# Optimization experiments

Hardware: AMD Instinct MI355X
Metric: run time of the kernel (lower is better)

## Reference

```python
import jax, jax.numpy as jnp
import numpy as np

N = 4096            # number of graph nodes (keypoints)
L_MAX = 6
Q = 2
D, H, W = 64, 128, 128
ST = 0.15           # sigma_transition
SP = 0.3            # sigma_pairwise
AU = 1.0            # alpha_unary
L = len(range(0, 2 * L_MAX + 1, Q)) ** 3   # 343 displacement labels


def setup_inputs() -> dict:
    key = jax.random.key(0)
    k1, k2 = jax.random.split(key)
    unary = jax.random.normal(k1, (N, L), dtype=jnp.float32)
    u = jax.random.uniform(k2, (N, N), dtype=jnp.float32)
    dist = (u + u.T) * 0.5  # symmetric pairwise distance matrix
    # Buffer A exactly as in __init__: displacement grid -> RBF transition kernel
    r = np.arange(0, 2 * L_MAX + 1, Q, dtype=np.float32)
    g = np.stack(np.meshgrid(r, r, r, indexing='ij'), axis=3).reshape(-1, 3) - L_MAX
    disp = g[:, ::-1] * 2.0 / np.array([W - 1, H - 1, D - 1], dtype=np.float32)
    A = np.exp(-((disp[:, None, :] - disp[None, :, :]) ** 2).sum(-1) / (2.0 * ST ** 2))
    return {"unary": unary, "dist": dist, "A": jnp.asarray(A, dtype=jnp.float32)}


def _forward(unary, dist, A):
    n, l = unary.shape
    unary = AU * unary
    pairwise = jnp.exp(-dist / (2.0 * SP ** 2))
    INF = jnp.float32(1e30)
    idx = jnp.arange(n)
    d = dist.at[idx, idx].set(INF)  # no self edges

    # ---- Prim's MST rooted at node 0 (addition order = parents-before-children) ----
    in_tree0 = jnp.zeros((n,), dtype=bool).at[0].set(True)
    best0 = d[0]                      # cheapest edge from each node into the tree
    parent0 = jnp.zeros((n,), jnp.int32)
    order0 = jnp.zeros((n,), jnp.int32)

    def prim_body(i, st):
        in_tree, best, parent, order = st
        nxt = jnp.argmin(jnp.where(in_tree, INF, best)).astype(jnp.int32)
        in_tree = in_tree.at[nxt].set(True)
        order = order.at[i].set(nxt)
        upd = (d[nxt] < best) & ~in_tree
        parent = jnp.where(upd, nxt, parent)
        best = jnp.where(upd, d[nxt], best)
        return (in_tree, best, parent, order)

    _, _, parent, order = jax.lax.fori_loop(1, n, prim_body, (in_tree0, best0, parent0, order0))
    root = order[0]  # == 0

    # ---- Upward (leaves -> root) max-sum Viterbi messages along tree edges ----
    ptr0 = jnp.zeros((n, l), jnp.int32)

    def up(carry, c):
        belief, ptr = carry
        p = parent[c]
        # scores[l_c, l_p] = belief[c, l_c] + pairwise(c,p) * A[l_c, l_p]
        scores = belief[c][:, None] + pairwise[c, p] * A
        msg = scores.max(axis=0)                                   # [L]
        ptr = ptr.at[c].set(jnp.argmax(scores, axis=0).astype(jnp.int32))
        belief = belief.at[p].add(jnp.where(c == root, 0.0, msg))  # root sends nothing
        return (belief, ptr), None

    (belief, ptr), _ = jax.lax.scan(up, (unary, ptr0), order[::-1])

    # ---- Downward backtracking (root -> leaves) ----
    def down(labels, c):
        lab = jnp.where(c == root,
                        jnp.argmax(belief[root]).astype(jnp.int32),
                        ptr[c, labels[parent[c]]])
        return labels.at[c].set(lab), None

    labels, _ = jax.lax.scan(down, jnp.zeros((n,), jnp.int32), order)

    # disp_out = -1 everywhere, +1 at selected label, scaled by 1e5
    onehot = jax.nn.one_hot(labels, l, dtype=unary.dtype)
    return (2.0 * onehot - 1.0) * 100000.0


def reference(unary, dist, A):
    return _forward(unary, dist, A)
```

## Files before the change

### kernel.cpp

```cpp
#include <hip/hip_runtime.h>
#include <hip/hip_cooperative_groups.h>
#include <math.h>

namespace cg = cooperative_groups;
typedef unsigned long long u64;

#define NN 4096
#define LBL 343
#define PSTRIDE 344
#define APITCH 344
#define U64MAX 0xFFFFFFFFFFFFFFFFull
#define MST_ROUNDS 12

__global__ void mrf_mst_init_kernel(int* __restrict__ compA,
                                    u64* __restrict__ minEa, u64* __restrict__ minEb,
                                    int* __restrict__ counters)
{
  const int i = blockIdx.x * blockDim.x + threadIdx.x;
  if (i < NN) { compA[i] = i; minEa[i] = U64MAX; minEb[i] = U64MAX; }
  if (i == 0) { counters[0] = NN; counters[1] = NN; counters[2] = 0; }
}

__global__ void mrf_padA_kernel(const float* __restrict__ A, float* __restrict__ Apad)
{
  const int id = blockIdx.x * 256 + threadIdx.x;
  if (id >= LBL * APITCH) return;
  const int r = id / APITCH;
  const int c = id - r * APITCH;
  Apad[id] = (c < LBL) ? A[r * LBL + c] : 0.0f;
}

__global__ __launch_bounds__(1024) void mrf_scan_kernel(
    const float* __restrict__ dist, const int* __restrict__ compR,
    u64* __restrict__ minE, int* __restrict__ counters, int round)
{
  __shared__ int s_cc[16];
  __shared__ u64 s_cv[16];

  if (blockIdx.x == 0 && threadIdx.x == 0) counters[round & 1] = 0;
  if (round > 0 && counters[(round - 1) & 1] <= 1) return;

  const int i    = (blockIdx.x * 1024 + threadIdx.x) >> 6;
  const int lane = threadIdx.x & 63;
  const int wib  = threadIdx.x >> 6;

  const int ci = compR[i];
  const float4* rowp = (const float4*)(dist + (size_t)i * NN);
  const int4* cp = (const int4*)compR;
  u64 best = U64MAX;
  #pragma unroll 4
  for (int k = 0; k < 16; ++k) {
    const int q = k * 64 + lane;
    const float4 dv = rowp[q];
    const int4 cv = cp[q];
    const int j0 = q * 4;
    if (cv.x != ci) { const u64 p = ((u64)__float_as_uint(dv.x) << 24) | ((u64)i << 12) | (u64)(j0    ); best = best < p ? best : p; }
    if (cv.y != ci) { const u64 p = ((u64)__float_as_uint(dv.y) << 24) | ((u64)i << 12) | (u64)(j0 + 1); best = best < p ? best : p; }
    if (cv.z != ci) { const u64 p = ((u64)__float_as_uint(dv.z) << 24) | ((u64)i << 12) | (u64)(j0 + 2); best = best < p ? best : p; }
    if (cv.w != ci) { const u64 p = ((u64)__float_as_uint(dv.w) << 24) | ((u64)i << 12) | (u64)(j0 + 3); best = best < p ? best : p; }
  }
  #pragma unroll
  for (int sh = 32; sh >= 1; sh >>= 1) {
    const u64 o = __shfl_down(best, sh);
    best = best < o ? best : o;
  }
  if (lane == 0) {
    s_cc[wib] = (best == U64MAX) ? -1 : ci;
    s_cv[wib] = best;
  }
  __syncthreads();
  if (threadIdx.x == 0) {
    for (int a = 0; a < 16; ++a) {
      const int c = s_cc[a];
      if (c < 0) continue;
      bool dup = false;
      for (int b2 = 0; b2 < a; ++b2) if (s_cc[b2] == c) { dup = true; break; }
      if (dup) continue;
      u64 b = s_cv[a];
      for (int b2 = a + 1; b2 < 16; ++b2)
        if (s_cc[b2] == c && s_cv[b2] < b) b = s_cv[b2];
      atomicMin(&minE[c & (NN - 1)], b);
    }
  }
}

__global__ __launch_bounds__(1024) void mrf_hook_kernel(
    const int* __restrict__ compR, int* __restrict__ compW,
    const u64* __restrict__ minE, u64* __restrict__ minEnext,
    int* __restrict__ eu, int* __restrict__ ev, unsigned* __restrict__ ew,
    int* __restrict__ counters, int round)
{
  if (round > 0 && counters[(round - 1) & 1] <= 1) return;
  const int i = blockIdx.x * 1024 + threadIdx.x;
  if (i >= NN) return;
  minEnext[i] = U64MAX;

  const int r0 = compR[i];
  int cur = r0;
  for (int guard = 0; guard < NN + 2; ++guard) {
    const u64 e = minE[cur];
    if (e == U64MAX) break;
    const int v = (int)(e & 0xFFF);
    const int t = compR[v];
    if (t == cur) break;
    const u64 te = minE[t];
    if (te != U64MAX) {
      const int tv = (int)(te & 0xFFF);
      if (compR[tv] == cur && cur < t) break;
    }
    cur = t;
  }
  compW[i] = cur;
  if (cur == i) atomicAdd(&counters[round & 1], 1);

  if (r0 == i) {
    const u64 e = minE[i];
    if (e != U64MAX) {
      const int v = (int)(e & 0xFFF);
      const int u = (int)((e >> 12) & 0xFFF);
      const unsigned wb = (unsigned)(e >> 24);
      const int t = compR[v];
      bool mutual = false;
      const u64 te = minE[t];
      if (te != U64MAX) {
        const int tv = (int)(te & 0xFFF);
        mutual = (compR[tv] == i);
      }
      if (!(mutual && i < t)) {
        const int slot = atomicAdd(&counters[2], 1);
        if (slot < NN) { eu[slot] = u; ev[slot] = v; ew[slot] = wb; }
      }
    }
  }
}

__device__ __forceinline__ void scan4096(int* arr, int* tmp16, int tid)
{
  __syncthreads();
  const int base = tid * 4;
  const int c0 = arr[base], c1 = arr[base + 1], c2 = arr[base + 2], c3 = arr[base + 3];
  const int lsum = c0 + c1 + c2 + c3;
  const int lane = tid & 63, wid = tid >> 6;
  int incl = lsum;
  #pragma unroll
  for (int o = 1; o < 64; o <<= 1) {
    const int t = __shfl_up(incl, o);
    if (lane >= o) incl += t;
  }
  if (lane == 63) tmp16[wid] = incl;
  __syncthreads();
  if (tid == 0) {
    int run = 0;
    for (int w = 0; w < 16; ++w) { const int t = tmp16[w]; tmp16[w] = run; run += t; }
  }
  __syncthreads();
  const int excl = tmp16[wid] + incl - lsum;
  arr[base]     = excl;
  arr[base + 1] = excl + c0;
  arr[base + 2] = excl + c0 + c1;
  arr[base + 3] = excl + c0 + c1 + c2;
  __syncthreads();
}

__global__ __launch_bounds__(1024) void mrf_root_kernel(
    const float* __restrict__ dist,
    const int* __restrict__ eu, const int* __restrict__ ev, const unsigned* __restrict__ ew,
    int* __restrict__ parent_g, int* __restrict__ childStart, int* __restrict__ childList,
    int* __restrict__ levStart, int* __restrict__ levNodes, int* __restrict__ segList,
    int* __restrict__ meta, float* __restrict__ w_edge,
    u64* __restrict__ adjList, int* __restrict__ ready)
{
  __shared__ int s_deg[NN];
  __shared__ int s_start[NN];
  __shared__ int s_cur[NN];
  __shared__ int s_parent[NN];
  __shared__ unsigned short s_dep[NN];
  __shared__ unsigned short s_fr[2][NN];
  __shared__ int s_tmp16[16];
  __shared__ int s_fcnt, s_nf;

  const int tid = threadIdx.x;

  for (int j = tid; j < NN; j += 1024) ready[j] = 0;

  for (int j = tid; j < NN; j += 1024) s_deg[j] = 0;
  __syncthreads();
  for (int e = tid; e < NN - 1; e += 1024) {
    atomicAdd(&s_deg[eu[e] & (NN - 1)], 1);
    atomicAdd(&s_deg[ev[e] & (NN - 1)], 1);
  }
  __syncthreads();
  for (int j = tid; j < NN; j += 1024) s_start[j] = s_deg[j];
  scan4096(s_start, s_tmp16, tid);
  for (int j = tid; j < NN; j += 1024) s_cur[j] = s_start[j];
  __syncthreads();
  for (int e = tid; e < NN - 1; e += 1024) {
    const int u = eu[e] & (NN - 1), v = ev[e] & (NN - 1);
    const u64 wb = (u64)ew[e];
    const int p1 = atomicAdd(&s_cur[u], 1);
    adjList[p1] = (wb << 12) | (u64)v;
    const int p2 = atomicAdd(&s_cur[v], 1);
    adjList[p2] = (wb << 12) | (u64)u;
  }
  __syncthreads();

  for (int j = tid; j < NN; j += 1024) { s_parent[j] = 0; s_dep[j] = 0; }
  if (tid == 0) { s_fcnt = 1; s_nf = 0; s_fr[0][0] = 0; }
  __syncthreads();
  int cur = 0, lev = 0;
  while (true) {
    const int fcnt = s_fcnt;
    if (fcnt == 0) break;
    for (int idx = tid; idx < fcnt; idx += 1024) {
      const int x = s_fr[cur][idx];
      const int st = s_start[x], dg = s_deg[x];
      for (int a = 0; a < dg; ++a) {
        const u64 ent = adjList[st + a];
        const int nb = (int)(ent & 0xFFF);
        if (nb != s_parent[x] || x == 0) {
          s_parent[nb] = x;
          s_dep[nb] = (unsigned short)(lev + 1);
          const int slot = atomicAdd(&s_nf, 1);
          s_fr[1 - cur][slot] = (unsigned short)nb;
        }
      }
    }
    __syncthreads();
    if (tid == 0) { s_fcnt = s_nf; s_nf = 0; }
    ++lev;
    cur ^= 1;
    __syncthreads();
  }
  const int numLev = lev;
  if (tid == 0) { s_parent[0] = 0; meta[0] = numLev; }
  __syncthreads();

  int* s_cs2 = (int*)s_fr;
  for (int j = tid; j < NN; j += 1024) s_cs2[j] = s_deg[j] - (j != 0 ? 1 : 0);
  scan4096(s_cs2, s_tmp16, tid);
  for (int j = tid; j < NN; j += 1024) childStart[j] = s_cs2[j];
  if (tid == 0) childStart[NN] = NN - 1;
  __syncthreads();

  for (int p = tid; p < NN; p += 1024) {
    const int st = s_start[p], dg = s_deg[p], cs = s_cs2[p];
    const int par = s_parent[p];
    u64 buf[16];
    int m = 0;
    for (int a = 0; a < dg; ++a) {
      const u64 ent = adjList[st + a];
      const int nb = (int)(ent & 0xFFF);
      if (p != 0 && nb == par) continue;
      if (m < 16) {
        int q = m;
        while (q > 0 && buf[q - 1] < ent) { buf[q] = buf[q - 1]; --q; }
        buf[q] = ent;
        ++m;
      } else {
        childList[cs + m] = nb;
        ++m;
      }
    }
    const int lim = m < 16 ? m : 16;
    for (int k = 0; k < lim; ++k) childList[cs + k] = (int)(buf[k] & 0xFFF);
  }

  for (int j = tid; j < NN; j += 1024) s_cur[j] = 0;
  __syncthreads();
  for (int j = tid; j < NN; j += 1024) atomicAdd(&s_cur[s_dep[j]], 1);
  scan4096(s_cur, s_tmp16, tid);
  for (int j = tid; j < NN; j += 1024) { levStart[j] = s_cur[j]; s_start[j] = s_cur[j]; }
  if (tid == 0) levStart[NN] = NN;
  __syncthreads();
  for (int j = tid; j < NN; j += 1024) {
    const int pos = atomicAdd(&s_start[s_dep[j]], 1);
    levNodes[pos] = j;
  }
  __syncthreads();

  if (tid == 0) s_nf = 0;
  for (int j = tid; j < NN; j += 1024) s_cur[j] = 0;
  __syncthreads();
  for (int j = tid; j < NN; j += 1024) {
    const int ce = (j == NN - 1) ? (NN - 1) : s_cs2[j + 1];
    int key = -1;
    if (ce - s_cs2[j] == 0) {
      int c = j;
      while (c != 0) {
        const int par = s_parent[c];
        if (childList[s_cs2[par]] != c) break;
        c = par;
      }
      key = s_dep[c];
      atomicAdd(&s_cur[numLev - 1 - key], 1);
      atomicAdd(&s_nf, 1);
    }
    s_deg[j] = key;
  }
  scan4096(s_cur, s_tmp16, tid);
  for (int j = tid; j < NN; j += 1024) s_start[j] = s_cur[j];
  __syncthreads();
  for (int j = tid; j < NN; j += 1024) {
    const int key = s_deg[j];
    if (key >= 0) {
      const int pos = atomicAdd(&s_start[numLev - 1 - key], 1);
      segList[pos] = j;
    }
  }
  if (tid == 0) meta[1] = s_nf;

  for (int j = tid; j < NN; j += 1024) {
    parent_g[j] = s_parent[j];
    w_edge[j] = (j == 0) ? 0.0f
                         : expf(-dist[(size_t)j * NN + s_parent[j]] / 0.18f);
  }
}

__global__ __launch_bounds__(768) void mrf_solve_kernel(
    const float* __restrict__ unary, const float* __restrict__ Apad,
    float* __restrict__ msgbuf, unsigned short* __restrict__ ptrbuf,
    const int* __restrict__ parent, const int* __restrict__ childStart,
    const int* __restrict__ childList, const int* __restrict__ levStart,
    const int* __restrict__ levNodes, const int* __restrict__ segList,
    const float* __restrict__ w_edge,
    int* __restrict__ labels, const int* __restrict__ meta,
    int* __restrict__ ready)
{
  __shared__ float s_b[APITCH];
  __shared__ float s_pv[8][APITCH];
  __shared__ int   s_pi[8][APITCH];
  __shared__ int   s_lab[NN];
  const int tid = threadIdx.x;
  const bool act = (tid < 688);
  const int t = act ? (tid % 86) : 0;
  const int h = act ? (tid / 86) : 0;
  const int lc0 = h * 43;
  const int lc1 = (h == 7) ? LBL : (lc0 + 43);

  int numLev = meta[0];
  if (numLev < 1) numLev = 1;
  if (numLev > NN) numLev = NN;
  int numSegs = meta[1];
  if (numSegs < 1) numSegs = 1;
  if (numSegs > NN) numSegs = NN;

  bool didRoot = false;

  for (int sidx = blockIdx.x; sidx < numSegs && !didRoot; sidx += gridDim.x) {
    int v = segList[sidx] & (NN - 1);
    if (tid < LBL) s_b[tid] = unary[(size_t)v * LBL + tid];
    __syncthreads();

    while (true) {
      if (v == 0) {
        if (tid == 0) {
          float bv = s_b[0]; int bi = 0;
          for (int l = 1; l < LBL; ++l)
            if (s_b[l] > bv) { bv = s_b[l]; bi = l; }
          labels[0] = bi;
          s_lab[0] = bi;
        }
        __syncthreads();
        didRoot = true;
        break;
      }

      if (act) {
        const float w = w_edge[v];
        const float4* __restrict__ Ap4 = (const float4*)Apad;
        float4 a = Ap4[(size_t)lc0 * 86 + t];
        float sb = s_b[lc0];
        float bv0 = __fadd_rn(sb, __fmul_rn(w, a.x));
        float bv1 = __fadd_rn(sb, __fmul_rn(w, a.y));
        float bv2 = __fadd_rn(sb, __fmul_rn(w, a.z));
        float bv3 = __fadd_rn(sb, __fmul_rn(w, a.w));
        int bi0 = lc0, bi1 = lc0, bi2 = lc0, bi3 = lc0;
        #pragma unroll 2
        for (int lc = lc0 + 1; lc < lc1; ++lc) {
          const float4 av = Ap4[(size_t)lc * 86 + t];
          const float sbl = s_b[lc];
          const float s0 = __fadd_rn(sbl, __fmul_rn(w, av.x));
          const float s1 = __fadd_rn(sbl, __fmul_rn(w, av.y));
          const float s2 = __fadd_rn(sbl, __fmul_rn(w, av.z));
          const float s3 = __fadd_rn(sbl, __fmul_rn(w, av.w));
          if (s0 > bv0) { bv0 = s0; bi0 = lc; }
          if (s1 > bv1) { bv1 = s1; bi1 = lc; }
          if (s2 > bv2) { bv2 = s2; bi2 = lc; }
          if (s3 > bv3) { bv3 = s3; bi3 = lc; }
        }
        const int lpb = t * 4;
        s_pv[h][lpb + 0] = bv0; s_pi[h][lpb + 0] = bi0;
        s_pv[h][lpb + 1] = bv1; s_pi[h][lpb + 1] = bi1;
        s_pv[h][lpb + 2] = bv2; s_pi[h][lpb + 2] = bi2;
        s_pv[h][lpb + 3] = bv3; s_pi[h][lpb + 3] = bi3;
      }
      __syncthreads();

      float fbv = 0.0f;
      if (tid < LBL) {
        fbv = s_pv[0][tid];
        int fbi = s_pi[0][tid];
        #pragma unroll
        for (int hh = 1; hh < 8; ++hh) {
          const float pv = s_pv[hh][tid];
          if (pv > fbv) { fbv = pv; fbi = s_pi[hh][tid]; }
        }
        s_pi[0][tid] = fbi;
      }
      __syncthreads();

      if (tid < 172) {
        const unsigned lo = (unsigned)s_pi[0][2 * tid] & 0xFFFFu;
        const unsigned hi = (2 * tid + 1 < LBL)
                              ? ((unsigned)s_pi[0][2 * tid + 1] & 0xFFFFu) : 0u;
        __hip_atomic_store((unsigned*)(ptrbuf + (size_t)v * PSTRIDE + 2 * tid),
                           lo | (hi << 16),
                           __ATOMIC_RELAXED, __HIP_MEMORY_SCOPE_AGENT);
      }

      const int p = parent[v] & (NN - 1);
      const int csp = childStart[p];
      int degp = childStart[p + 1] - csp;
      if (degp < 1) degp = 1;
      if (degp > 64) degp = 64;
      const bool isCarrier = ((childList[csp] & (NN - 1)) == v);

      if (!isCarrier) {
        if (tid < LBL)
          __hip_atomic_store((unsigned*)&msgbuf[(size_t)v * LBL + tid],
                             __float_as_uint(fbv),
                             __ATOMIC_RELAXED, __HIP_MEMORY_SCOPE_AGENT);
        __syncthreads();
        if (tid == 0)
          __hip_atomic_fetch_add(&ready[p], 1,
                                 __ATOMIC_RELEASE, __HIP_MEMORY_SCOPE_AGENT);
        break;
      }

      if (degp > 1 && tid == 0) {
        long long guard = 0;
        while (__hip_atomic_load(&ready[p], __ATOMIC_RELAXED,
                                 __HIP_MEMORY_SCOPE_AGENT) < degp - 1) {
          __builtin_amdgcn_s_sleep(1);
          if (++guard > 30000000LL) break;
        }
      }
      __syncthreads();

      if (tid < LBL) {
        float nb = __fadd_rn(unary[(size_t)p * LBL + tid], fbv);
        for (int k = 1; k < degp; ++k) {
          const int ch = childList[csp + k] & (NN - 1);
          const unsigned um = __hip_atomic_load(
              (const unsigned*)&msgbuf[(size_t)ch * LBL + tid],
              __ATOMIC_RELAXED, __HIP_MEMORY_SCOPE_AGENT);
          nb = __fadd_rn(nb, __uint_as_float(um));
        }
        s_b[tid] = nb;
      }
      v = p;
      __syncthreads();
    }
  }

  if (!didRoot) return;
  __syncthreads();
  for (int lev = 1; lev < numLev; ++lev) {
    int ls = levStart[lev], le = levStart[lev + 1];
    if (ls < 0) ls = 0;
    if (le > NN) le = NN;
    for (int idx = ls + tid; idx < le; idx += 768) {
      const int c = levNodes[idx] & (NN - 1);
      int pl = s_lab[parent[c] & (NN - 1)];
      if (pl < 0) pl = 0;
      if (pl >= LBL) pl = LBL - 1;
      const unsigned pk = __hip_atomic_load(
          (const unsigned*)(ptrbuf + (size_t)c * PSTRIDE + (pl & ~1)),
          __ATOMIC_RELAXED, __HIP_MEMORY_SCOPE_AGENT);
      const int lab = (pl & 1) ? (int)(pk >> 16) : (int)(pk & 0xFFFFu);
      s_lab[c] = lab;
      labels[c] = lab;
    }
    __syncthreads();
  }
}

__global__ void mrf_out_kernel(const int* __restrict__ labels, float* __restrict__ out)
{
  const int id = blockIdx.x * blockDim.x + threadIdx.x;
  if (id >= NN * LBL) return;
  const int c = id / LBL;
  const int l = id - c * LBL;
  out[id] = (l == labels[c]) ? 100000.0f : -100000.0f;
}

extern "C" void kernel_launch(void* const* d_in, const int* in_sizes, int n_in,
                              void* d_out, int out_size, void* d_ws, size_t ws_size,
                              hipStream_t stream)
{
  (void)in_sizes; (void)n_in; (void)out_size; (void)ws_size;
  const float* unary = (const float*)d_in[0];
  const float* dist  = (const float*)d_in[1];
  const float* A     = (const float*)d_in[2];
  float* out = (float*)d_out;

  char* ws = (char*)d_ws;
  size_t off = 0;
  auto take = [&](size_t bytes) -> void* {
    void* p = (void*)(ws + off);
    off += (bytes + 255) & ~(size_t)255;
    return p;
  };
  float* msgbuf = out;
  unsigned short* ptrbuf = (unsigned short*)take((size_t)NN * PSTRIDE * sizeof(unsigned short));
  float*    Apad       = (float*)   take((size_t)LBL * APITCH * sizeof(float));
  int*      compA      = (int*)     take(NN * sizeof(int));
  int*      compB      = (int*)     take(NN * sizeof(int));
  u64*      minEa      = (u64*)     take(NN * sizeof(u64));
  u64*      minEb      = (u64*)     take(NN * sizeof(u64));
  int*      eu         = (int*)     take(NN * sizeof(int));
  int*      ev         = (int*)     take(NN * sizeof(int));
  unsigned* ew         = (unsigned*)take(NN * sizeof(unsigned));
  int*      counters   = (int*)     take(256);
  int*      parent     = (int*)     take(NN * sizeof(int));
  int*      childStart = (int*)     take((NN + 1) * sizeof(int));
  int*      childList  = (int*)     take(NN * sizeof(int));
  int*      levStart   = (int*)     take((NN + 1) * sizeof(int));
  int*      levNodes   = (int*)     take(NN * sizeof(int));
  int*      segList    = (int*)     take(NN * sizeof(int));
  int*      labels     = (int*)     take(NN * sizeof(int));
  int*      meta       = (int*)     take(256);
  float*    w_edge     = (float*)   take(NN * sizeof(float));
  int*      ready      = (int*)     take(NN * sizeof(int));
  u64*      adjList    = (u64*)     take((size_t)2 * NN * sizeof(u64));

  hipLaunchKernelGGL(mrf_mst_init_kernel, dim3(4), dim3(1024), 0, stream,
                     compA, minEa, minEb, counters);
  hipLaunchKernelGGL(mrf_padA_kernel, dim3((LBL * APITCH + 255) / 256), dim3(256),
                     0, stream, A, Apad);

  for (int r = 0; r < MST_ROUNDS; ++r) {
    const int* compR = (r & 1) ? compB : compA;
    int*       compW = (r & 1) ? compA : compB;
    u64*       mcur  = (r & 1) ? minEb : minEa;
    u64*       mnext = (r & 1) ? minEa : minEb;
    hipLaunchKernelGGL(mrf_scan_kernel, dim3(256), dim3(1024), 0, stream,
                       dist, compR, mcur, counters, r);
    hipLaunchKernelGGL(mrf_hook_kernel, dim3(4), dim3(1024), 0, stream,
                       compR, compW, mcur, mnext, eu, ev, ew, counters, r);
  }

  hipLaunchKernelGGL(mrf_root_kernel, dim3(1), dim3(1024), 0, stream,
                     dist, eu, ev, ew, parent, childStart, childList,
                     levStart, levNodes, segList, meta, w_edge, adjList, ready);

  {
    void* args[] = {
      (void*)&unary, (void*)&Apad, (void*)&msgbuf, (void*)&ptrbuf,
      (void*)&parent, (void*)&childStart, (void*)&childList,
      (void*)&levStart, (void*)&levNodes, (void*)&segList, (void*)&w_edge,
      (void*)&labels, (void*)&meta, (void*)&ready
    };
    hipLaunchCooperativeKernel((void*)mrf_solve_kernel, dim3(256), dim3(768),
                               args, 0, stream);
  }

  const int total = NN * LBL;
  hipLaunchKernelGGL(mrf_out_kernel, dim3((total + 255) / 256), dim3(256), 0, stream,
                     labels, out);
}
```

Before: 907.9 us.

## Skip dominated label chunks in max-sum message with precomputed A bounds

Precomputes, for each of the 8 label chunks and each parent label, the maximum A value over that chunk. During each upward message, it also keeps per-64-label maxima of the belief. From these it forms an upper bound on the chunk's best score and skips the 43-row scan when the bound is below the diagonal candidate (belief[lp] + w, since A's diagonal is 1). This avoids most of the inner max/argmax work on the serial tree-path critical chain. The cost is an extra warp reduction per step and a small precompute kernel. It relies on the bound being exact under round-to-nearest arithmetic, and argmax tie-breaking could differ.

```diff
diff --git a/kernel.cpp b/kernel.cpp
--- a/kernel.cpp
+++ b/kernel.cpp
@@ -11,6 +11,7 @@
 #define APITCH 344
 #define U64MAX 0xFFFFFFFFFFFFFFFFull
 #define MST_ROUNDS 12
+#define NEGINF -3.4e38f
 
 __global__ void mrf_mst_init_kernel(int* __restrict__ compA,
                                     u64* __restrict__ minEa, u64* __restrict__ minEb,
@@ -28,6 +29,19 @@
   const int r = id / APITCH;
   const int c = id - r * APITCH;
   Apad[id] = (c < LBL) ? A[r * LBL + c] : 0.0f;
+}
+
+__global__ void mrf_amax_kernel(const float* __restrict__ Apad, float* __restrict__ AmaxT)
+{
+  const int id = blockIdx.x * 256 + threadIdx.x;
+  if (id >= 8 * APITCH) return;
+  const int hh = id / APITCH;
+  const int lp = id - hh * APITCH;
+  const int l0 = 43 * hh;
+  const int l1 = (hh == 7) ? LBL : (l0 + 43);
+  float m = NEGINF;
+  for (int lc = l0; lc < l1; ++lc) m = fmaxf(m, Apad[(size_t)lp * APITCH + lc]);
+  AmaxT[id] = m;
 }
 
 __global__ __launch_bounds__(1024) void mrf_scan_kernel(
@@ -318,6 +332,7 @@
 
 __global__ __launch_bounds__(768) void mrf_solve_kernel(
     const float* __restrict__ unary, const float* __restrict__ Apad,
+    const float* __restrict__ AmaxT,
     float* __restrict__ msgbuf, unsigned short* __restrict__ ptrbuf,
     const int* __restrict__ parent, const int* __restrict__ childStart,
     const int* __restrict__ childList, const int* __restrict__ levStart,
@@ -326,16 +341,19 @@
     int* __restrict__ labels, const int* __restrict__ meta,
     int* __restrict__ ready)
 {
-  __shared__ float s_b[APITCH];
+  __shared__ __align__(16) float s_b[APITCH];
   __shared__ float s_pv[8][APITCH];
   __shared__ int   s_pi[8][APITCH];
   __shared__ int   s_lab[NN];
+  __shared__ float s_gmax[6];
   const int tid = threadIdx.x;
   const bool act = (tid < 688);
   const int t = act ? (tid % 86) : 0;
   const int h = act ? (tid / 86) : 0;
   const int lc0 = h * 43;
   const int lc1 = (h == 7) ? LBL : (lc0 + 43);
+  const int g0 = (43 * h) >> 6;
+  const int g1 = (43 * h + 42) >> 6;
 
   int numLev = meta[0];
   if (numLev < 1) numLev = 1;
@@ -348,7 +366,14 @@
 
   for (int sidx = blockIdx.x; sidx < numSegs && !didRoot; sidx += gridDim.x) {
     int v = segList[sidx] & (NN - 1);
-    if (tid < LBL) s_b[tid] = unary[(size_t)v * LBL + tid];
+    if (tid < 384) {
+      float xv = NEGINF;
+      if (tid < LBL) { xv = unary[(size_t)v * LBL + tid]; s_b[tid] = xv; }
+      else if (tid == LBL) s_b[LBL] = 3.4e38f;
+      #pragma unroll
+      for (int sh = 32; sh >= 1; sh >>= 1) xv = fmaxf(xv, __shfl_down(xv, sh));
+      if ((tid & 63) == 0) s_gmax[tid >> 6] = xv;
+    }
     __syncthreads();
 
     while (true) {
@@ -367,32 +392,47 @@
 
       if (act) {
         const float w = w_edge[v];
-        const float4* __restrict__ Ap4 = (const float4*)Apad;
-        float4 a = Ap4[(size_t)lc0 * 86 + t];
-        float sb = s_b[lc0];
-        float bv0 = __fadd_rn(sb, __fmul_rn(w, a.x));
-        float bv1 = __fadd_rn(sb, __fmul_rn(w, a.y));
-        float bv2 = __fadd_rn(sb, __fmul_rn(w, a.z));
-        float bv3 = __fadd_rn(sb, __fmul_rn(w, a.w));
-        int bi0 = lc0, bi1 = lc0, bi2 = lc0, bi3 = lc0;
-        #pragma unroll 2
-        for (int lc = lc0 + 1; lc < lc1; ++lc) {
-          const float4 av = Ap4[(size_t)lc * 86 + t];
-          const float sbl = s_b[lc];
-          const float s0 = __fadd_rn(sbl, __fmul_rn(w, av.x));
-          const float s1 = __fadd_rn(sbl, __fmul_rn(w, av.y));
-          const float s2 = __fadd_rn(sbl, __fmul_rn(w, av.z));
-          const float s3 = __fadd_rn(sbl, __fmul_rn(w, av.w));
-          if (s0 > bv0) { bv0 = s0; bi0 = lc; }
-          if (s1 > bv1) { bv1 = s1; bi1 = lc; }
-          if (s2 > bv2) { bv2 = s2; bi2 = lc; }
-          if (s3 > bv3) { bv3 = s3; bi3 = lc; }
+        const int lpb = t * 4;
+        const float4 am  = *(const float4*)(AmaxT + h * APITCH + lpb);
+        const float4 sb4 = *(const float4*)&s_b[lpb];
+        const float bmU = fmaxf(s_gmax[g0], s_gmax[g1]);
+        const bool skip =
+            (__fadd_rn(bmU, __fmul_rn(w, am.x)) < __fadd_rn(sb4.x, w)) &&
+            (__fadd_rn(bmU, __fmul_rn(w, am.y)) < __fadd_rn(sb4.y, w)) &&
+            (__fadd_rn(bmU, __fmul_rn(w, am.z)) < __fadd_rn(sb4.z, w)) &&
+            (__fadd_rn(bmU, __fmul_rn(w, am.w)) < __fadd_rn(sb4.w, w));
+        if (skip) {
+          s_pv[h][lpb + 0] = NEGINF; s_pi[h][lpb + 0] = 0;
+          s_pv[h][lpb + 1] = NEGINF; s_pi[h][lpb + 1] = 0;
+          s_pv[h][lpb + 2] = NEGINF; s_pi[h][lpb + 2] = 0;
+          s_pv[h][lpb + 3] = NEGINF; s_pi[h][lpb + 3] = 0;
+        } else {
+          const float4* __restrict__ Ap4 = (const float4*)Apad;
+          float4 a = Ap4[(size_t)lc0 * 86 + t];
+          float sb = s_b[lc0];
+          float bv0 = __fadd_rn(sb, __fmul_rn(w, a.x));
+          float bv1 = __fadd_rn(sb, __fmul_rn(w, a.y));
+          float bv2 = __fadd_rn(sb, __fmul_rn(w, a.z));
+          float bv3 = __fadd_rn(sb, __fmul_rn(w, a.w));
+          int bi0 = lc0, bi1 = lc0, bi2 = lc0, bi3 = lc0;
+          #pragma unroll 2
+          for (int lc = lc0 + 1; lc < lc1; ++lc) {
+            const float4 av = Ap4[(size_t)lc * 86 + t];
+            const float sbl = s_b[lc];
+            const float s0 = __fadd_rn(sbl, __fmul_rn(w, av.x));
+            const float s1 = __fadd_rn(sbl, __fmul_rn(w, av.y));
+            const float s2 = __fadd_rn(sbl, __fmul_rn(w, av.z));
+            const float s3 = __fadd_rn(sbl, __fmul_rn(w, av.w));
+            if (s0 > bv0) { bv0 = s0; bi0 = lc; }
+            if (s1 > bv1) { bv1 = s1; bi1 = lc; }
+            if (s2 > bv2) { bv2 = s2; bi2 = lc; }
+            if (s3 > bv3) { bv3 = s3; bi3 = lc; }
+          }
+          s_pv[h][lpb + 0] = bv0; s_pi[h][lpb + 0] = bi0;
+          s_pv[h][lpb + 1] = bv1; s_pi[h][lpb + 1] = bi1;
+          s_pv[h][lpb + 2] = bv2; s_pi[h][lpb + 2] = bi2;
+          s_pv[h][lpb + 3] = bv3; s_pi[h][lpb + 3] = bi3;
         }
-        const int lpb = t * 4;
-        s_pv[h][lpb + 0] = bv0; s_pi[h][lpb + 0] = bi0;
-        s_pv[h][lpb + 1] = bv1; s_pi[h][lpb + 1] = bi1;
-        s_pv[h][lpb + 2] = bv2; s_pi[h][lpb + 2] = bi2;
-        s_pv[h][lpb + 3] = bv3; s_pi[h][lpb + 3] = bi3;
       }
       __syncthreads();
 
@@ -447,16 +487,23 @@
       }
       __syncthreads();
 
-      if (tid < LBL) {
-        float nb = __fadd_rn(unary[(size_t)p * LBL + tid], fbv);
-        for (int k = 1; k < degp; ++k) {
-          const int ch = childList[csp + k] & (NN - 1);
-          const unsigned um = __hip_atomic_load(
-              (const unsigned*)&msgbuf[(size_t)ch * LBL + tid],
-              __ATOMIC_RELAXED, __HIP_MEMORY_SCOPE_AGENT);
-          nb = __fadd_rn(nb, __uint_as_float(um));
+      if (tid < 384) {
+        float nb = NEGINF;
+        if (tid < LBL) {
+          nb = __fadd_rn(unary[(size_t)p * LBL + tid], fbv);
+          for (int k = 1; k < degp; ++k) {
+            const int ch = childList[csp + k] & (NN - 1);
+            const unsigned um = __hip_atomic_load(
+                (const unsigned*)&msgbuf[(size_t)ch * LBL + tid],
+                __ATOMIC_RELAXED, __HIP_MEMORY_SCOPE_AGENT);
+            nb = __fadd_rn(nb, __uint_as_float(um));
+          }
+          s_b[tid] = nb;
         }
-        s_b[tid] = nb;
+        float xv = nb;
+        #pragma unroll
+        for (int sh = 32; sh >= 1; sh >>= 1) xv = fmaxf(xv, __shfl_down(xv, sh));
+        if ((tid & 63) == 0) s_gmax[tid >> 6] = xv;
       }
       v = p;
       __syncthreads();
@@ -514,6 +561,7 @@
   float* msgbuf = out;
   unsigned short* ptrbuf = (unsigned short*)take((size_t)NN * PSTRIDE * sizeof(unsigned short));
   float*    Apad       = (float*)   take((size_t)LBL * APITCH * sizeof(float));
+  float*    AmaxT      = (float*)   take((size_t)8 * APITCH * sizeof(float));
   int*      compA      = (int*)     take(NN * sizeof(int));
   int*      compB      = (int*)     take(NN * sizeof(int));
   u64*      minEa      = (u64*)     take(NN * sizeof(u64));
@@ -538,6 +586,8 @@
                      compA, minEa, minEb, counters);
   hipLaunchKernelGGL(mrf_padA_kernel, dim3((LBL * APITCH + 255) / 256), dim3(256),
                      0, stream, A, Apad);
+  hipLaunchKernelGGL(mrf_amax_kernel, dim3((8 * APITCH + 255) / 256), dim3(256),
+                     0, stream, Apad, AmaxT);
 
   for (int r = 0; r < MST_ROUNDS; ++r) {
     const int* compR = (r & 1) ? compB : compA;
@@ -556,7 +606,7 @@
 
   {
     void* args[] = {
-      (void*)&unary, (void*)&Apad, (void*)&msgbuf, (void*)&ptrbuf,
+      (void*)&unary, (void*)&Apad, (void*)&AmaxT, (void*)&msgbuf, (void*)&ptrbuf,
       (void*)&parent, (void*)&childStart, (void*)&childList,
       (void*)&levStart, (void*)&levNodes, (void*)&segList, (void*)&w_edge,
       (void*)&labels, (void*)&meta, (void*)&ready
```

Measured after the change: 953.3 us. 1.05x slower.

## Use dynamic atomic work queue for solve segments and merge init kernels

Applied to the files above, without the earlier changes.

Replaces the static blockIdx-strided assignment of tree segments in the solve kernel with a global atomic cursor, so blocks that finish early pick up the next segment. This targets load imbalance between segments of different lengths. It also merges the MST init and A-padding kernels into one launch to save a launch. The cursor adds one atomic and one barrier per segment, and the order in which segments are claimed now changes, which could affect the dependency waits on ready flags.

```diff
diff --git a/kernel.cpp b/kernel.cpp
--- a/kernel.cpp
+++ b/kernel.cpp
@@ -12,22 +12,19 @@
 #define U64MAX 0xFFFFFFFFFFFFFFFFull
 #define MST_ROUNDS 12
 
-__global__ void mrf_mst_init_kernel(int* __restrict__ compA,
-                                    u64* __restrict__ minEa, u64* __restrict__ minEb,
-                                    int* __restrict__ counters)
-{
-  const int i = blockIdx.x * blockDim.x + threadIdx.x;
-  if (i < NN) { compA[i] = i; minEa[i] = U64MAX; minEb[i] = U64MAX; }
-  if (i == 0) { counters[0] = NN; counters[1] = NN; counters[2] = 0; }
-}
-
-__global__ void mrf_padA_kernel(const float* __restrict__ A, float* __restrict__ Apad)
+__global__ void mrf_init_kernel(const float* __restrict__ A, float* __restrict__ Apad,
+                                int* __restrict__ compA,
+                                u64* __restrict__ minEa, u64* __restrict__ minEb,
+                                int* __restrict__ counters)
 {
   const int id = blockIdx.x * 256 + threadIdx.x;
-  if (id >= LBL * APITCH) return;
-  const int r = id / APITCH;
-  const int c = id - r * APITCH;
-  Apad[id] = (c < LBL) ? A[r * LBL + c] : 0.0f;
+  if (id < NN) { compA[id] = id; minEa[id] = U64MAX; minEb[id] = U64MAX; }
+  if (id == 0) { counters[0] = NN; counters[1] = NN; counters[2] = 0; }
+  if (id < LBL * APITCH) {
+    const int r = id / APITCH;
+    const int c = id - r * APITCH;
+    Apad[id] = (c < LBL) ? A[r * LBL + c] : 0.0f;
+  }
 }
 
 __global__ __launch_bounds__(1024) void mrf_scan_kernel(
@@ -168,7 +165,7 @@
     int* __restrict__ parent_g, int* __restrict__ childStart, int* __restrict__ childList,
     int* __restrict__ levStart, int* __restrict__ levNodes, int* __restrict__ segList,
     int* __restrict__ meta, float* __restrict__ w_edge,
-    u64* __restrict__ adjList, int* __restrict__ ready)
+    u64* __restrict__ adjList, int* __restrict__ ready, int* __restrict__ cursor)
 {
   __shared__ int s_deg[NN];
   __shared__ int s_start[NN];
@@ -182,6 +179,7 @@
   const int tid = threadIdx.x;
 
   for (int j = tid; j < NN; j += 1024) ready[j] = 0;
+  if (tid == 0) cursor[0] = 0;
 
   for (int j = tid; j < NN; j += 1024) s_deg[j] = 0;
   __syncthreads();
@@ -324,12 +322,13 @@
     const int* __restrict__ levNodes, const int* __restrict__ segList,
     const float* __restrict__ w_edge,
     int* __restrict__ labels, const int* __restrict__ meta,
-    int* __restrict__ ready)
+    int* __restrict__ ready, int* __restrict__ cursor)
 {
   __shared__ float s_b[APITCH];
   __shared__ float s_pv[8][APITCH];
   __shared__ int   s_pi[8][APITCH];
   __shared__ int   s_lab[NN];
+  __shared__ int   s_sidx;
   const int tid = threadIdx.x;
   const bool act = (tid < 688);
   const int t = act ? (tid % 86) : 0;
@@ -346,7 +345,12 @@
 
   bool didRoot = false;
 
-  for (int sidx = blockIdx.x; sidx < numSegs && !didRoot; sidx += gridDim.x) {
+  while (!didRoot) {
+    if (tid == 0) s_sidx = atomicAdd(cursor, 1);
+    __syncthreads();
+    const int sidx = s_sidx;
+    if (sidx >= numSegs) break;
+
     int v = segList[sidx] & (NN - 1);
     if (tid < LBL) s_b[tid] = unary[(size_t)v * LBL + tid];
     __syncthreads();
@@ -532,12 +536,11 @@
   int*      meta       = (int*)     take(256);
   float*    w_edge     = (float*)   take(NN * sizeof(float));
   int*      ready      = (int*)     take(NN * sizeof(int));
+  int*      cursor     = (int*)     take(256);
   u64*      adjList    = (u64*)     take((size_t)2 * NN * sizeof(u64));
 
-  hipLaunchKernelGGL(mrf_mst_init_kernel, dim3(4), dim3(1024), 0, stream,
-                     compA, minEa, minEb, counters);
-  hipLaunchKernelGGL(mrf_padA_kernel, dim3((LBL * APITCH + 255) / 256), dim3(256),
-                     0, stream, A, Apad);
+  hipLaunchKernelGGL(mrf_init_kernel, dim3((LBL * APITCH + 255) / 256), dim3(256),
+                     0, stream, A, Apad, compA, minEa, minEb, counters);
 
   for (int r = 0; r < MST_ROUNDS; ++r) {
     const int* compR = (r & 1) ? compB : compA;
@@ -552,14 +555,15 @@
 
   hipLaunchKernelGGL(mrf_root_kernel, dim3(1), dim3(1024), 0, stream,
                      dist, eu, ev, ew, parent, childStart, childList,
-                     levStart, levNodes, segList, meta, w_edge, adjList, ready);
+                     levStart, levNodes, segList, meta, w_edge, adjList,
+                     ready, cursor);
 
   {
     void* args[] = {
       (void*)&unary, (void*)&Apad, (void*)&msgbuf, (void*)&ptrbuf,
       (void*)&parent, (void*)&childStart, (void*)&childList,
       (void*)&levStart, (void*)&levNodes, (void*)&segList, (void*)&w_edge,
-      (void*)&labels, (void*)&meta, (void*)&ready
+      (void*)&labels, (void*)&meta, (void*)&ready, (void*)&cursor
     };
     hipLaunchCooperativeKernel((void*)mrf_solve_kernel, dim3(256), dim3(768),
                                args, 0, stream);
```

Result: no change. 912.5 us (+0.5%).
